# Optimization experiments

Measured on AMD Instinct MI355X. Metric: run time of the kernel, lower is better.

The kernel has to match this reference:

```python
import jax, jax.numpy as jnp
import numpy as np

VOCAB = 32000
EMB = 512
STATE = 512
B = 4
S = 1024


def setup_inputs() -> dict:
    key = jax.random.key(0)
    ks = jax.random.split(key, 6)
    x = jax.random.randint(ks[0], (B, S), 0, VOCAB)
    emb_table = jax.random.normal(ks[1], (VOCAB, EMB), dtype=jnp.float32)
    a = jax.random.normal(ks[2], (STATE, STATE), dtype=jnp.float32) * 0.02
    b = jax.random.normal(ks[3], (EMB, STATE), dtype=jnp.float32) * 0.02
    # nn.Linear(state, vocab): weight [vocab, state], bias [vocab]
    lim = 1.0 / np.sqrt(STATE)
    c_w = jax.random.uniform(ks[4], (VOCAB, STATE), minval=-lim, maxval=lim, dtype=jnp.float32)
    c_b = jax.random.uniform(ks[5], (VOCAB,), minval=-lim, maxval=lim, dtype=jnp.float32)
    return {"x": x, "emb_table": emb_table, "a": a, "b": b, "c_w": c_w, "c_b": c_b}


def reference(x, emb_table, a, b, c_w, c_b):
    emb = emb_table[x]                      # [B, S, E]
    # Precompute input projection for all timesteps (single GEMM).
    u = jnp.einsum('bse,en->bsn', emb, b)   # [B, S, N]
    u_t = jnp.swapaxes(u, 0, 1)             # [S, B, N] for scan

    def step(state, u_step):
        new_state = jnp.tanh(state @ a + u_step)  # [B, N]
        return new_state, new_state

    init = jnp.zeros((x.shape[0], a.shape[0]), dtype=emb.dtype)
    _, states = jax.lax.scan(step, init, u_t)   # states: [S, B, N]
    # Readout (dropout=0 -> identity). One big GEMM over all timesteps.
    logits = jnp.einsum('sbn,vn->sbv', states, c_w) + c_b  # [S, B, V]
    return jnp.swapaxes(logits, 0, 1)           # [B, S, V]
```

## Files before the change

kernel.cpp:

```cpp
#include <hip/hip_runtime.h>
#include <hip/hip_fp16.h>

typedef _Float16 f16;
typedef _Float16 f16x8 __attribute__((ext_vector_type(8)));
typedef _Float16 f16x4 __attribute__((ext_vector_type(4)));
typedef float f32x4v __attribute__((ext_vector_type(4)));
typedef unsigned long long u64;

#define S_LEN 1024
#define NS 512
#define NV 32000
#define NW 4
#define SENT 0x7C007C007C007C00ULL
#define FUSED_LDS 98304

#define MFMA16(a, b, c) __builtin_amdgcn_mfma_f32_16x16x32_f16((a), (b), (c), 0, 0, 0)


__global__ __launch_bounds__(256) void transpose512_f16_kernel(
        const float* __restrict__ src, f16* __restrict__ dstT,
        u64* __restrict__ X) {
    int idx = blockIdx.x * 256 + threadIdx.x;
    X[idx] = SENT;
    X[idx + 262144] = SENT;
    int r = idx >> 9;
    int c = idx & 511;
    dstT[c * 512 + r] = (f16)src[idx];
}

__global__ __launch_bounds__(256) void embu_kernel(
        const int* __restrict__ x, const float* __restrict__ emb,
        const f16* __restrict__ bT, f16* __restrict__ u16) {
    __shared__ f16 embA[64 * 40];
    __shared__ f16 Bt[512 * 40];
    __shared__ int xi[64];

    int t = threadIdx.x;
    int wg = blockIdx.x;
    if (t < 64) {
        int m = wg * 64 + t;
        int bb = m & 3, ss = m >> 2;
        xi[t] = x[bb * S_LEN + ss];
    }
    __syncthreads();

    int wv = t >> 6, l = t & 63, lr = l & 15, lg = l >> 4;

    f32x4v acc[32];
#pragma unroll
    for (int i = 0; i < 32; i++) acc[i] = (f32x4v){0.f, 0.f, 0.f, 0.f};

    for (int kc = 0; kc < 512; kc += 32) {
        __syncthreads();
        {
            int tk = t >> 2, c0 = (t & 3) * 8;
            const float* src = emb + (size_t)xi[tk] * NS + kc + c0;
            float4 v0 = *(const float4*)src;
            float4 v1 = *(const float4*)(src + 4);
            f16x8 h;
            h[0] = (f16)v0.x; h[1] = (f16)v0.y; h[2] = (f16)v0.z; h[3] = (f16)v0.w;
            h[4] = (f16)v1.x; h[5] = (f16)v1.y; h[6] = (f16)v1.z; h[7] = (f16)v1.w;
            *(f16x8*)&embA[tk * 40 + c0] = h;
        }
        {
            int c0 = (t & 3) * 8;
            int n0 = t >> 2;
#pragma unroll
            for (int rr = 0; rr < 8; rr++) {
                int n = rr * 64 + n0;
                f16x8 v = *(const f16x8*)&bT[n * 512 + kc + c0];
                *(f16x8*)&Bt[n * 40 + c0] = v;
            }
        }
        __syncthreads();

        f16x8 af = *(const f16x8*)&embA[(wv * 16 + lr) * 40 + 8 * lg];
#pragma unroll
        for (int vt = 0; vt < 32; vt++) {
            f16x8 bf = *(const f16x8*)&Bt[(vt * 16 + lr) * 40 + 8 * lg];
            acc[vt] = MFMA16(af, bf, acc[vt]);
        }
    }

    int m0 = wg * 64 + wv * 16 + 4 * lg;
    int ss = m0 >> 2;
#pragma unroll
    for (int vt = 0; vt < 32; vt++) {
        int n = vt * 16 + lr;
        f16x4 h;
#pragma unroll
        for (int i = 0; i < 4; i++) h[i] = (f16)acc[vt][i];
        *(f16x4*)&u16[((size_t)ss * NS + n) * 4] = h;
    }
}

__global__ __launch_bounds__(512) void fused_kernel(
        const float* __restrict__ a, const f16* __restrict__ u16,
        const float* __restrict__ cw, const float* __restrict__ cb,
        u64* __restrict__ X, float* __restrict__ out) {
    extern __shared__ char smem[];
    int t = threadIdx.x;
    int bid = blockIdx.x;
    int w = t >> 6, l = t & 63, lr = l & 15, lg = l >> 4;

    if (bid < NW) {
        f16* Sb = (f16*)smem;
        int r = bid;
        int col = r * 128 + w * 16 + lr;

        int gcol = -1;
        if (w < 6) {
            int cwk = w + (w >= 2 * r ? 2 : 0);
            gcol = cwk * 64 + l;
        }

        for (int i = t; i < 2 * 4 * 544; i += 512) Sb[i] = (f16)0.f;

        f16x8 afr[16];
#pragma unroll
        for (int ks = 0; ks < 16; ks++) {
            f16x8 h;
#pragma unroll
            for (int j = 0; j < 8; j++)
                h[j] = (f16)a[(size_t)(ks * 32 + 8 * lg + j) * NS + col];
            afr[ks] = h;
        }

        f16x4 upf = *(const f16x4*)&u16[(size_t)col * 4];

        __syncthreads();

#pragma unroll 1
        for (int s = 0; s < S_LEN; s++) {
            int cur = s & 1, nxt = cur ^ 1;

            f32x4v acca, accb;
            acca[0] = (float)upf[0]; acca[1] = (float)upf[1];
            acca[2] = (float)upf[2]; acca[3] = (float)upf[3];
            accb = (f32x4v){0.f, 0.f, 0.f, 0.f};

            {
                int sn = (s + 1 < S_LEN) ? s + 1 : S_LEN - 1;
                upf = *(const f16x4*)&u16[((size_t)sn * NS + col) * 4];
            }

            const char* sb = (const char*)Sb + cur * 4352 +
                             (lr & 3) * 1088 + lg * 16;
#pragma unroll
            for (int ks = 0; ks < 16; ks += 2) {
                f16x8 s0 = *(const f16x8*)(sb + ks * 64);
                f16x8 s1 = *(const f16x8*)(sb + ks * 64 + 64);
                acca = MFMA16(s0, afr[ks], acca);
                accb = MFMA16(s1, afr[ks + 1], accb);
            }

            if (lg == 0) {
                union { u64 u; f16 h[4]; } pk;
#pragma unroll
                for (int i = 0; i < 4; i++) {
                    float y = acca[i] + accb[i];
                    float e = __expf(2.0f * y);
                    float rc = __builtin_amdgcn_rcpf(e + 1.0f);
                    y = __builtin_fmaf(-2.0f, rc, 1.0f);
                    pk.h[i] = (f16)y;
                }
                __hip_atomic_store(&X[(size_t)s * NS + col], pk.u,
                                   __ATOMIC_RELAXED, __HIP_MEMORY_SCOPE_AGENT);
#pragma unroll
                for (int i = 0; i < 4; i++)
                    Sb[nxt * 2176 + i * 544 + col] = pk.h[i];
            }

            if (s == S_LEN - 1) break;

            if (w < 6) {
                u64 v;
                do {
                    v = __hip_atomic_load(&X[(size_t)s * NS + gcol],
                                          __ATOMIC_RELAXED,
                                          __HIP_MEMORY_SCOPE_AGENT);
                } while (v == SENT);
                union { u64 u; f16 h[4]; } pk;
                pk.u = v;
#pragma unroll
                for (int i = 0; i < 4; i++)
                    Sb[nxt * 2176 + i * 544 + gcol] = pk.h[i];
            }

            asm volatile("s_waitcnt lgkmcnt(0)" ::: "memory");
            __builtin_amdgcn_s_barrier();
            __builtin_amdgcn_sched_barrier(0);
        }
        return;
    }

    f16* Ast = (f16*)smem;
    f16* Bw = (f16*)(smem + 256 * 72 * 2);

    int idx = bid - NW;
    int bm = idx / 250;
    int bn = idx % 250;
    int s0 = bm * 64;

    if (t == 0) {
        int sc = (bm == 15) ? (S_LEN - 1) : (s0 + 64);
        while (__hip_atomic_load(&X[(size_t)sc * NS], __ATOMIC_RELAXED,
                                 __HIP_MEMORY_SCOPE_AGENT) == SENT)
            __builtin_amdgcn_s_sleep(16);
    }
    __syncthreads();

    int wr = w >> 1, wc = w & 1;

    f32x4v acc[4][4];
#pragma unroll
    for (int i = 0; i < 4; i++)
#pragma unroll
        for (int j = 0; j < 4; j++) acc[i][j] = (f32x4v){0.f, 0.f, 0.f, 0.f};

    for (int kc = 0; kc < 512; kc += 64) {
        __syncthreads();
        {
            int srel = t >> 3;
            int ck = (t & 7) * 8;
            const u64* xs = &X[(size_t)(s0 + srel) * NS + kc + ck];
            u64 v[8];
#pragma unroll
            for (int j = 0; j < 8; j++) v[j] = xs[j];
#pragma unroll
            for (int j = 0; j < 8; j++)
                while (v[j] == SENT)
                    v[j] = __hip_atomic_load(&xs[j], __ATOMIC_RELAXED,
                                             __HIP_MEMORY_SCOPE_AGENT);
#pragma unroll
            for (int b = 0; b < 4; b++) {
                f16x8 row;
#pragma unroll
                for (int j = 0; j < 8; j++) {
                    union { u64 u; f16 h[4]; } pk;
                    pk.u = v[j];
                    row[j] = pk.h[b];
                }
                *(f16x8*)&Ast[(srel * 4 + b) * 72 + ck] = row;
            }
        }
#pragma unroll
        for (int q = 0; q < 4; q++) {
            int i2 = q * 512 + t;
            int row = i2 >> 4;
            int c0 = (i2 & 15) * 4;
            float4 v = *(const float4*)&cw[(size_t)(bn * 128 + row) * NS + kc + c0];
            f16x4 h;
            h[0] = (f16)v.x; h[1] = (f16)v.y; h[2] = (f16)v.z; h[3] = (f16)v.w;
            *(f16x4*)&Bw[row * 72 + c0] = h;
        }
        __syncthreads();

#pragma unroll
        for (int ks = 0; ks < 2; ks++) {
            f16x8 af[4], bf[4];
#pragma unroll
            for (int mt = 0; mt < 4; mt++)
                af[mt] = *(const f16x8*)&Ast[(wr * 64 + mt * 16 + lr) * 72 +
                                             ks * 32 + 8 * lg];
#pragma unroll
            for (int vt = 0; vt < 4; vt++)
                bf[vt] = *(const f16x8*)&Bw[(wc * 64 + vt * 16 + lr) * 72 +
                                            ks * 32 + 8 * lg];
#pragma unroll
            for (int mt = 0; mt < 4; mt++)
#pragma unroll
                for (int vt = 0; vt < 4; vt++)
                    acc[mt][vt] = MFMA16(af[mt], bf[vt], acc[mt][vt]);
        }
    }

    float bias[4];
#pragma unroll
    for (int vt = 0; vt < 4; vt++)
        bias[vt] = cb[bn * 128 + wc * 64 + vt * 16 + lr];

#pragma unroll
    for (int mt = 0; mt < 4; mt++) {
#pragma unroll
        for (int i = 0; i < 4; i++) {
            int m = bm * 256 + wr * 64 + mt * 16 + 4 * lg + i;
            int bb = m & 3, ss = m >> 2;
            float* orow = out + (size_t)(bb * S_LEN + ss) * NV + bn * 128 + wc * 64;
#pragma unroll
            for (int vt = 0; vt < 4; vt++)
                orow[vt * 16 + lr] = acc[mt][vt][i] + bias[vt];
        }
    }
}

extern "C" void kernel_launch(void* const* d_in, const int* in_sizes, int n_in,
                              void* d_out, int out_size, void* d_ws, size_t ws_size,
                              hipStream_t stream) {
    (void)in_sizes; (void)n_in; (void)out_size; (void)ws_size;

    const int*   x   = (const int*)d_in[0];
    const float* emb = (const float*)d_in[1];
    const float* a   = (const float*)d_in[2];
    const float* bm  = (const float*)d_in[3];
    const float* cw  = (const float*)d_in[4];
    const float* cb  = (const float*)d_in[5];
    float* out = (float*)d_out;

    char* ws = (char*)d_ws;
    f16* u16 = (f16*)(ws);
    u64* X   = (u64*)(ws + (4u << 20));
    f16* bT16 = (f16*)(ws + (8u << 20));

    hipFuncSetAttribute(reinterpret_cast<const void*>(fused_kernel),
                        hipFuncAttributeMaxDynamicSharedMemorySize,
                        FUSED_LDS);

    transpose512_f16_kernel<<<1024, 256, 0, stream>>>(bm, bT16, X);
    embu_kernel<<<64, 256, 0, stream>>>(x, emb, bT16, u16);
    fused_kernel<<<NW + 16 * 250, 512, FUSED_LDS, stream>>>(
        a, u16, cw, cb, X, out);
}
```

Baseline: 1.325 ms.

## Specialize recurrence waves into compute and gather roles; swizzle GEMM LDS tiles

Result: slower. 1.462 ms (+10.4%).

```diff
diff --git a/kernel.cpp b/kernel.cpp
--- a/kernel.cpp
+++ b/kernel.cpp
@@ -13,8 +13,11 @@
 #define NW 4
 #define SENT 0x7C007C007C007C00ULL
 #define FUSED_LDS 98304
+#define TPB 896
 
 #define MFMA16(a, b, c) __builtin_amdgcn_mfma_f32_16x16x32_f16((a), (b), (c), 0, 0, 0)
+
+#define XLD(p) __hip_atomic_load((p), __ATOMIC_RELAXED, __HIP_MEMORY_SCOPE_AGENT)
 
 
 __global__ __launch_bounds__(256) void transpose512_f16_kernel(
@@ -94,7 +97,7 @@
     }
 }
 
-__global__ __launch_bounds__(512) void fused_kernel(
+__global__ __launch_bounds__(TPB) void fused_kernel(
         const float* __restrict__ a, const f16* __restrict__ u16,
         const float* __restrict__ cw, const float* __restrict__ cb,
         u64* __restrict__ X, float* __restrict__ out) {
@@ -106,96 +109,117 @@
     if (bid < NW) {
         f16* Sb = (f16*)smem;
         int r = bid;
-        int col = r * 128 + w * 16 + lr;
-
-        int gcol = -1;
-        if (w < 6) {
-            int cwk = w + (w >= 2 * r ? 2 : 0);
-            gcol = cwk * 64 + l;
-        }
-
-        for (int i = t; i < 2 * 4 * 544; i += 512) Sb[i] = (f16)0.f;
-
-        f16x8 afr[16];
-#pragma unroll
-        for (int ks = 0; ks < 16; ks++) {
-            f16x8 h;
-#pragma unroll
-            for (int j = 0; j < 8; j++)
-                h[j] = (f16)a[(size_t)(ks * 32 + 8 * lg + j) * NS + col];
-            afr[ks] = h;
-        }
-
-        f16x4 upf = *(const f16x4*)&u16[(size_t)col * 4];
-
-        __syncthreads();
+
+        for (int i = t; i < 2 * 4 * 544; i += TPB) Sb[i] = (f16)0.f;
+
+        if (w < 8) {
+            int col = r * 128 + w * 16 + lr;
+
+            f16x8 afr[16];
+#pragma unroll
+            for (int ks = 0; ks < 16; ks++) {
+                f16x8 h;
+#pragma unroll
+                for (int j = 0; j < 8; j++)
+                    h[j] = (f16)a[(size_t)(ks * 32 + 8 * lg + j) * NS + col];
+                afr[ks] = h;
+            }
+
+            f16x4 upf = *(const f16x4*)&u16[(size_t)col * 4];
+
+            __syncthreads();
 
 #pragma unroll 1
-        for (int s = 0; s < S_LEN; s++) {
-            int cur = s & 1, nxt = cur ^ 1;
-
-            f32x4v acca, accb;
-            acca[0] = (float)upf[0]; acca[1] = (float)upf[1];
-            acca[2] = (float)upf[2]; acca[3] = (float)upf[3];
-            accb = (f32x4v){0.f, 0.f, 0.f, 0.f};
-
-            {
-                int sn = (s + 1 < S_LEN) ? s + 1 : S_LEN - 1;
-                upf = *(const f16x4*)&u16[((size_t)sn * NS + col) * 4];
-            }
-
-            const char* sb = (const char*)Sb + cur * 4352 +
-                             (lr & 3) * 1088 + lg * 16;
-#pragma unroll
-            for (int ks = 0; ks < 16; ks += 2) {
-                f16x8 s0 = *(const f16x8*)(sb + ks * 64);
-                f16x8 s1 = *(const f16x8*)(sb + ks * 64 + 64);
-                acca = MFMA16(s0, afr[ks], acca);
-                accb = MFMA16(s1, afr[ks + 1], accb);
-            }
-
-            if (lg == 0) {
-                union { u64 u; f16 h[4]; } pk;
-#pragma unroll
-                for (int i = 0; i < 4; i++) {
-                    float y = acca[i] + accb[i];
-                    float e = __expf(2.0f * y);
-                    float rc = __builtin_amdgcn_rcpf(e + 1.0f);
-                    y = __builtin_fmaf(-2.0f, rc, 1.0f);
-                    pk.h[i] = (f16)y;
-                }
-                __hip_atomic_store(&X[(size_t)s * NS + col], pk.u,
-                                   __ATOMIC_RELAXED, __HIP_MEMORY_SCOPE_AGENT);
-#pragma unroll
-                for (int i = 0; i < 4; i++)
-                    Sb[nxt * 2176 + i * 544 + col] = pk.h[i];
-            }
-
-            if (s == S_LEN - 1) break;
-
-            if (w < 6) {
+            for (int s = 0; s < S_LEN; s++) {
+                int cur = s & 1, nxt = cur ^ 1;
+
+                f32x4v acca, accb;
+                acca[0] = (float)upf[0]; acca[1] = (float)upf[1];
+                acca[2] = (float)upf[2]; acca[3] = (float)upf[3];
+                accb = (f32x4v){0.f, 0.f, 0.f, 0.f};
+
+                {
+                    int sn = (s + 1 < S_LEN) ? s + 1 : S_LEN - 1;
+                    upf = *(const f16x4*)&u16[((size_t)sn * NS + col) * 4];
+                }
+
+                const char* sb = (const char*)Sb + cur * 4352 +
+                                 (lr & 3) * 1088 + lg * 16;
+#pragma unroll
+                for (int ks = 0; ks < 16; ks += 2) {
+                    f16x8 s0 = *(const f16x8*)(sb + ks * 64);
+                    f16x8 s1 = *(const f16x8*)(sb + ks * 64 + 64);
+                    acca = MFMA16(s0, afr[ks], acca);
+                    accb = MFMA16(s1, afr[ks + 1], accb);
+                }
+
+                if (lg == 0) {
+                    union { u64 u; f16 h[4]; } pk;
+#pragma unroll
+                    for (int i = 0; i < 4; i++) {
+                        float y = acca[i] + accb[i];
+                        float e = __expf(2.0f * y);
+                        float rc = __builtin_amdgcn_rcpf(e + 1.0f);
+                        y = __builtin_fmaf(-2.0f, rc, 1.0f);
+                        pk.h[i] = (f16)y;
+                    }
+                    __hip_atomic_store(&X[(size_t)s * NS + col], pk.u,
+                                       __ATOMIC_RELAXED,
+                                       __HIP_MEMORY_SCOPE_AGENT);
+                    if (s < S_LEN - 1) {
+#pragma unroll
+                        for (int i = 0; i < 4; i++)
+                            Sb[nxt * 2176 + i * 544 + col] = pk.h[i];
+                    }
+                }
+                if (s == S_LEN - 1) break;
+
+                asm volatile("s_waitcnt lgkmcnt(0)" ::: "memory");
+                __builtin_amdgcn_s_barrier();
+                __builtin_amdgcn_sched_barrier(0);
+            }
+        } else {
+            int gw = w - 8;
+            int cwk = gw + (gw >= 2 * r ? 2 : 0);
+            int gcol = cwk * 64 + l;
+
+            __syncthreads();
+
+#pragma unroll 1
+            for (int s = 0; s < S_LEN - 1; s++) {
+                int nxt = (s & 1) ^ 1;
+                const u64* p = &X[(size_t)s * NS + gcol];
+
                 u64 v;
-                do {
-                    v = __hip_atomic_load(&X[(size_t)s * NS + gcol],
-                                          __ATOMIC_RELAXED,
-                                          __HIP_MEMORY_SCOPE_AGENT);
-                } while (v == SENT);
+                u64 a0 = XLD(p), a1 = XLD(p), a2 = XLD(p), a3 = XLD(p);
+                for (;;) {
+                    if (a0 != SENT) { v = a0; break; }
+                    a0 = XLD(p);
+                    if (a1 != SENT) { v = a1; break; }
+                    a1 = XLD(p);
+                    if (a2 != SENT) { v = a2; break; }
+                    a2 = XLD(p);
+                    if (a3 != SENT) { v = a3; break; }
+                    a3 = XLD(p);
+                }
+                __builtin_amdgcn_sched_barrier(0);
+
                 union { u64 u; f16 h[4]; } pk;
                 pk.u = v;
 #pragma unroll
                 for (int i = 0; i < 4; i++)
                     Sb[nxt * 2176 + i * 544 + gcol] = pk.h[i];
-            }
-
-            asm volatile("s_waitcnt lgkmcnt(0)" ::: "memory");
-            __builtin_amdgcn_s_barrier();
-            __builtin_amdgcn_sched_barrier(0);
+
+                asm volatile("s_waitcnt lgkmcnt(0)" ::: "memory");
+                __builtin_amdgcn_s_barrier();
+                __builtin_amdgcn_sched_barrier(0);
+            }
         }
         return;
     }
 
-    f16* Ast = (f16*)smem;
-    f16* Bw = (f16*)(smem + 256 * 72 * 2);
+    char* AstB = smem;
+    char* BwB  = smem + 256 * 64 * 2;
 
     int idx = bid - NW;
     int bm = idx / 250;
@@ -203,9 +227,8 @@
     int s0 = bm * 64;
 
     if (t == 0) {
-        int sc = (bm == 15) ? (S_LEN - 1) : (s0 + 64);
-        while (__hip_atomic_load(&X[(size_t)sc * NS], __ATOMIC_RELAXED,
-                                 __HIP_MEMORY_SCOPE_AGENT) == SENT)
+        int sc = s0 + 56;
+        while (XLD(&X[(size_t)sc * NS]) == SENT)
             __builtin_amdgcn_s_sleep(16);
     }
     __syncthreads();
@@ -220,76 +243,89 @@
 
     for (int kc = 0; kc < 512; kc += 64) {
         __syncthreads();
-        {
-            int srel = t >> 3;
-            int ck = (t & 7) * 8;
-            const u64* xs = &X[(size_t)(s0 + srel) * NS + kc + ck];
-            u64 v[8];
-#pragma unroll
-            for (int j = 0; j < 8; j++) v[j] = xs[j];
-#pragma unroll
-            for (int j = 0; j < 8; j++)
-                while (v[j] == SENT)
-                    v[j] = __hip_atomic_load(&xs[j], __ATOMIC_RELAXED,
-                                             __HIP_MEMORY_SCOPE_AGENT);
-#pragma unroll
-            for (int b = 0; b < 4; b++) {
-                f16x8 row;
-#pragma unroll
-                for (int j = 0; j < 8; j++) {
-                    union { u64 u; f16 h[4]; } pk;
-                    pk.u = v[j];
-                    row[j] = pk.h[b];
-                }
-                *(f16x8*)&Ast[(srel * 4 + b) * 72 + ck] = row;
-            }
-        }
-#pragma unroll
-        for (int q = 0; q < 4; q++) {
-            int i2 = q * 512 + t;
-            int row = i2 >> 4;
-            int c0 = (i2 & 15) * 4;
-            float4 v = *(const float4*)&cw[(size_t)(bn * 128 + row) * NS + kc + c0];
-            f16x4 h;
-            h[0] = (f16)v.x; h[1] = (f16)v.y; h[2] = (f16)v.z; h[3] = (f16)v.w;
-            *(f16x4*)&Bw[row * 72 + c0] = h;
+        if (t < 512) {
+            {
+                int srel = t >> 3;
+                int ck = (t & 7) * 8;
+                const u64* xs = &X[(size_t)(s0 + srel) * NS + kc + ck];
+                u64 v[8];
+#pragma unroll
+                for (int j = 0; j < 8; j++) v[j] = xs[j];
+#pragma unroll
+                for (int j = 0; j < 8; j++)
+                    while (v[j] == SENT) v[j] = XLD(&xs[j]);
+#pragma unroll
+                for (int b = 0; b < 4; b++) {
+                    f16x8 row;
+#pragma unroll
+                    for (int j = 0; j < 8; j++) {
+                        union { u64 u; f16 h[4]; } pk;
+                        pk.u = v[j];
+                        row[j] = pk.h[b];
+                    }
+                    int rr = srel * 4 + b;
+                    int byte = (rr * 128 + ck * 2) ^ ((rr & 7) << 4);
+                    *(f16x8*)(AstB + byte) = row;
+                }
+            }
+#pragma unroll
+            for (int q = 0; q < 4; q++) {
+                int i2 = q * 512 + t;
+                int row = i2 >> 4;
+                int c0 = (i2 & 15) * 4;
+                float4 v = *(const float4*)&cw[(size_t)(bn * 128 + row) * NS +
+                                               kc + c0];
+                f16x4 h;
+                h[0] = (f16)v.x; h[1] = (f16)v.y; h[2] = (f16)v.z; h[3] = (f16)v.w;
+                int byte = (row * 128 + c0 * 2) ^ ((row & 7) << 4);
+                *(f16x4*)(BwB + byte) = h;
+            }
         }
         __syncthreads();
 
-#pragma unroll
-        for (int ks = 0; ks < 2; ks++) {
-            f16x8 af[4], bf[4];
-#pragma unroll
-            for (int mt = 0; mt < 4; mt++)
-                af[mt] = *(const f16x8*)&Ast[(wr * 64 + mt * 16 + lr) * 72 +
-                                             ks * 32 + 8 * lg];
-#pragma unroll
-            for (int vt = 0; vt < 4; vt++)
-                bf[vt] = *(const f16x8*)&Bw[(wc * 64 + vt * 16 + lr) * 72 +
-                                            ks * 32 + 8 * lg];
-#pragma unroll
-            for (int mt = 0; mt < 4; mt++)
+        if (w < 8) {
+#pragma unroll
+            for (int ks = 0; ks < 2; ks++) {
+                f16x8 af[4], bf[4];
+#pragma unroll
+                for (int mt = 0; mt < 4; mt++) {
+                    int rr = wr * 64 + mt * 16 + lr;
+                    int byte = (rr * 128 + ks * 64 + lg * 16) ^ ((lr & 7) << 4);
+                    af[mt] = *(const f16x8*)(AstB + byte);
+                }
+#pragma unroll
+                for (int vt = 0; vt < 4; vt++) {
+                    int rr = wc * 64 + vt * 16 + lr;
+                    int byte = (rr * 128 + ks * 64 + lg * 16) ^ ((lr & 7) << 4);
+                    bf[vt] = *(const f16x8*)(BwB + byte);
+                }
+#pragma unroll
+                for (int mt = 0; mt < 4; mt++)
+#pragma unroll
+                    for (int vt = 0; vt < 4; vt++)
+                        acc[mt][vt] = MFMA16(af[mt], bf[vt], acc[mt][vt]);
+            }
+        }
+    }
+
+    if (w < 8) {
+        float bias[4];
+#pragma unroll
+        for (int vt = 0; vt < 4; vt++)
+            bias[vt] = cb[bn * 128 + wc * 64 + vt * 16 + lr];
+
+#pragma unroll
+        for (int mt = 0; mt < 4; mt++) {
+#pragma unroll
+            for (int i = 0; i < 4; i++) {
+                int m = bm * 256 + wr * 64 + mt * 16 + 4 * lg + i;
+                int bb = m & 3, ss = m >> 2;
+                float* orow = out + (size_t)(bb * S_LEN + ss) * NV +
+                              bn * 128 + wc * 64;
 #pragma unroll
                 for (int vt = 0; vt < 4; vt++)
-                    acc[mt][vt] = MFMA16(af[mt], bf[vt], acc[mt][vt]);
-        }
-    }
-
-    float bias[4];
-#pragma unroll
-    for (int vt = 0; vt < 4; vt++)
-        bias[vt] = cb[bn * 128 + wc * 64 + vt * 16 + lr];
-
-#pragma unroll
-    for (int mt = 0; mt < 4; mt++) {
-#pragma unroll
-        for (int i = 0; i < 4; i++) {
-            int m = bm * 256 + wr * 64 + mt * 16 + 4 * lg + i;
-            int bb = m & 3, ss = m >> 2;
-            float* orow = out + (size_t)(bb * S_LEN + ss) * NV + bn * 128 + wc * 64;
-#pragma unroll
-            for (int vt = 0; vt < 4; vt++)
-                orow[vt * 16 + lr] = acc[mt][vt][i] + bias[vt];
+                    orow[vt * 16 + lr] = acc[mt][vt][i] + bias[vt];
+            }
         }
     }
 }
@@ -318,6 +354,6 @@
 
     transpose512_f16_kernel<<<1024, 256, 0, stream>>>(bm, bT16, X);
     embu_kernel<<<64, 256, 0, stream>>>(x, emb, bT16, u16);
-    fused_kernel<<<NW + 16 * 250, 512, FUSED_LDS, stream>>>(
+    fused_kernel<<<NW + 16 * 250, TPB, FUSED_LDS, stream>>>(
         a, u16, cw, cb, X, out);
 }
```
